# Performance work log

Measured on AMD Instinct MI355X. Metric: run time of the kernel, lower is better.

The kernel has to match this reference:

```python
import jax, jax.numpy as jnp
import numpy as np

N, E = 50000, 800000
IN_F, HID, HEADS, OUT_F = 128, 32, 4, 40
SLOPE = 0.2  # LeakyReLU negative slope (alpha)


def gatv2_layer(x, Wl, Wr, att, src, dst, n):
    # GATv2 (Brody et al.): score_ij = att . leakyrelu(Wl x_j + Wr x_i), message = Wl x_j
    H, F = att.shape
    gl = (x @ Wl).reshape(n, H, F)  # [N,H,F] source transform
    gr = (x @ Wr).reshape(n, H, F)  # [N,H,F] dest transform
    s = gl[src] + gr[dst]           # [E,H,F]
    e = jnp.where(s > 0, s, SLOPE * s)
    score = jnp.einsum('ehf,hf->eh', e, att)  # [E,H]
    m = jax.lax.stop_gradient(jax.ops.segment_max(score, dst, num_segments=n))
    a = jnp.exp(score - m[dst])
    denom = jax.ops.segment_sum(a, dst, num_segments=n)  # [N,H]
    w = a / (denom[dst] + 1e-16)                          # softmax over incoming edges
    out = jax.ops.segment_sum(w[:, :, None] * gl[src], dst, num_segments=n)  # [N,H,F]
    return out.reshape(n, H * F)


def setup_inputs() -> dict:
    key = jax.random.key(0)
    ks = jax.random.split(key, 12)
    d1 = HEADS * HID  # 128
    sc_in = 1.0 / np.sqrt(IN_F)
    sc_h = 1.0 / np.sqrt(d1)
    return {
        'x': jax.random.normal(ks[0], (N, IN_F), jnp.float32),
        'Wl1': jax.random.normal(ks[1], (IN_F, d1), jnp.float32) * sc_in,
        'Wr1': jax.random.normal(ks[2], (IN_F, d1), jnp.float32) * sc_in,
        'att1': jax.random.normal(ks[3], (HEADS, HID), jnp.float32) * (1.0 / np.sqrt(HID)),
        'Wl2': jax.random.normal(ks[4], (d1, d1), jnp.float32) * sc_h,
        'Wr2': jax.random.normal(ks[5], (d1, d1), jnp.float32) * sc_h,
        'att2': jax.random.normal(ks[6], (HEADS, HID), jnp.float32) * (1.0 / np.sqrt(HID)),
        'Wl3': jax.random.normal(ks[7], (d1, OUT_F), jnp.float32) * sc_h,
        'Wr3': jax.random.normal(ks[8], (d1, OUT_F), jnp.float32) * sc_h,
        'att3': jax.random.normal(ks[9], (1, OUT_F), jnp.float32) * (1.0 / np.sqrt(OUT_F)),
        'edge_index': jax.random.randint(ks[10], (2, E), 0, N, jnp.int64 if jax.config.jax_enable_x64 else jnp.int32),
    }


def reference(x, Wl1, Wr1, att1, Wl2, Wr2, att2, Wl3, Wr3, att3, edge_index):
    src, dst = edge_index[0], edge_index[1]
    h = jax.nn.elu(gatv2_layer(x, Wl1, Wr1, att1, src, dst, N))        # conv1 + ELU
    h = jax.nn.relu(gatv2_layer(h, Wl2, Wr2, att2, src, dst, N))       # hidden + ReLU (dropout off: eval)
    h = gatv2_layer(h, Wl3, Wr3, att3, src, dst, N)                    # conv2, 1 head
    return jax.nn.log_softmax(h, axis=1)
```

## Files before the change

### kernel.cpp

```cpp
#include <hip/hip_runtime.h>
#include <math.h>


#define TPB 256

typedef __attribute__((ext_vector_type(8))) short short8v;
typedef __attribute__((ext_vector_type(4))) float f32x4;

__device__ __forceinline__ short bf16rne(float v, float* recon) {
  unsigned u = __float_as_uint(v);
  unsigned r = (u + 0x7FFFu + ((u >> 16) & 1u)) >> 16;
  if (recon) *recon = __uint_as_float(r << 16);
  return (short)r;
}
__device__ __forceinline__ float bf2f(unsigned short u) {
  return __uint_as_float((unsigned)u << 16);
}

__global__ void k_prepW6(const float* __restrict__ s0, const float* __restrict__ s1,
                         const float* __restrict__ s2, const float* __restrict__ s3,
                         const float* __restrict__ s4, const float* __restrict__ s5,
                         short* __restrict__ wt) {
  int y = blockIdx.y;
  const float* W; short* hi; int M, Mp;
  if (y < 4) {
    W = (y == 0) ? s0 : (y == 1) ? s1 : (y == 2) ? s2 : s3;
    hi = wt + y * 32768; M = 128; Mp = 128;
  } else {
    W = (y == 4) ? s4 : s5;
    hi = wt + 131072 + (y - 4) * 12288; M = 40; Mp = 48;
  }
  short* lo = hi + 128 * Mp;
  int t = blockIdx.x * blockDim.x + threadIdx.x;
  if (t >= 128 * Mp) return;
  int m = t % Mp, k = t / Mp;
  float v = (m < M) ? W[k * M + m] : 0.f;
  float vh;
  short h = bf16rne(v, &vh);
  short l = bf16rne(v - vh, nullptr);
  hi[(size_t)m * 128 + k] = h;
  lo[(size_t)m * 128 + k] = l;
}

template <int ACT>
__device__ __forceinline__ void loadA(const float* __restrict__ x, int arow, int koff,
                                      short8v AH[4], short8v AL[4]) {
  const float4* px = reinterpret_cast<const float4*>(x + (size_t)arow * 128 + koff);
  float4 t[8];
#pragma unroll
  for (int k = 0; k < 4; ++k) {
    t[2 * k]     = px[k * 8];
    t[2 * k + 1] = px[k * 8 + 1];
  }
#pragma unroll
  for (int k = 0; k < 4; ++k) {
    float av[8] = {t[2 * k].x, t[2 * k].y, t[2 * k].z, t[2 * k].w,
                   t[2 * k + 1].x, t[2 * k + 1].y, t[2 * k + 1].z, t[2 * k + 1].w};
#pragma unroll
    for (int j = 0; j < 8; ++j) {
      float v = av[j];
      if (ACT == 1) v = v > 0.f ? v : (__expf(v) - 1.f);
      else if (ACT == 2) v = fmaxf(v, 0.f);
      float vh;
      AH[k][j] = bf16rne(v, &vh);
      AL[k][j] = bf16rne(v - vh, nullptr);
    }
  }
}

template <int ACT>
__global__ __launch_bounds__(256, 1) void k_gemm_mfma(
    const float* __restrict__ x,
    const short* __restrict__ blh, const short* __restrict__ bll,
    const short* __restrict__ brh, const short* __restrict__ brl,
    unsigned short* __restrict__ glh, float* __restrict__ gr, int n) {
  const int K = 128;
  int lane = threadIdx.x & 63;
  int w = threadIdx.x >> 6;
  int rbase = blockIdx.x * 64 + w * 16;
  int arow = rbase + (lane & 15);
  if (arow >= n) arow = n - 1;
  int koff = (lane >> 4) * 8;

  short8v AH[4], AL[4];
  loadA<ACT>(x, arow, koff, AH, AL);

  f32x4 acc[2][8];
#pragma unroll
  for (int m = 0; m < 2; ++m)
#pragma unroll
    for (int c = 0; c < 8; ++c) acc[m][c] = (f32x4)(0.f);

  int bbase = (lane & 15) * K + koff;

#define BOFF(IT) ((((IT) & 7) * 16 * K) + bbase + (((IT) >> 3) * 32))
  short8v cbh = *reinterpret_cast<const short8v*>(blh + BOFF(0));
  short8v cbl = *reinterpret_cast<const short8v*>(bll + BOFF(0));
  short8v cch = *reinterpret_cast<const short8v*>(brh + BOFF(0));
  short8v ccl = *reinterpret_cast<const short8v*>(brl + BOFF(0));
#pragma unroll
  for (int it = 0; it < 32; ++it) {
    const int k0i = it >> 3, c = it & 7;
    const int nit = (it + 1) & 31;
    short8v nbh = *reinterpret_cast<const short8v*>(blh + BOFF(nit));
    short8v nbl = *reinterpret_cast<const short8v*>(bll + BOFF(nit));
    short8v nch = *reinterpret_cast<const short8v*>(brh + BOFF(nit));
    short8v ncl = *reinterpret_cast<const short8v*>(brl + BOFF(nit));
    acc[0][c] = __builtin_amdgcn_mfma_f32_16x16x32_bf16(AH[k0i], cbh, acc[0][c], 0, 0, 0);
    acc[0][c] = __builtin_amdgcn_mfma_f32_16x16x32_bf16(AH[k0i], cbl, acc[0][c], 0, 0, 0);
    acc[0][c] = __builtin_amdgcn_mfma_f32_16x16x32_bf16(AL[k0i], cbh, acc[0][c], 0, 0, 0);
    acc[1][c] = __builtin_amdgcn_mfma_f32_16x16x32_bf16(AH[k0i], cch, acc[1][c], 0, 0, 0);
    acc[1][c] = __builtin_amdgcn_mfma_f32_16x16x32_bf16(AH[k0i], ccl, acc[1][c], 0, 0, 0);
    acc[1][c] = __builtin_amdgcn_mfma_f32_16x16x32_bf16(AL[k0i], cch, acc[1][c], 0, 0, 0);
    cbh = nbh; cbl = nbl; cch = nch; ccl = ncl;
  }
#undef BOFF

  int crow = rbase + (lane >> 4) * 4;
  int ccol = lane & 15;
#pragma unroll
  for (int c = 0; c < 8; ++c)
#pragma unroll
    for (int j = 0; j < 4; ++j) {
      int r = crow + j;
      if (r < n) {
        glh[(size_t)r * 128 + c * 16 + ccol] = (unsigned short)bf16rne(acc[0][c][j], nullptr);
        gr[(size_t)r * 128 + c * 16 + ccol] = acc[1][c][j];
      }
    }
}

template <int ACT>
__global__ __launch_bounds__(256, 1) void k_gemm_mfma3(
    const float* __restrict__ x,
    const short* __restrict__ blh, const short* __restrict__ bll,
    const short* __restrict__ brh, const short* __restrict__ brl,
    unsigned short* __restrict__ glh, float* __restrict__ gr, int n) {
  const int K = 128;
  int lane = threadIdx.x & 63;
  int w = threadIdx.x >> 6;
  int rbase = blockIdx.x * 64 + w * 16;
  int arow = rbase + (lane & 15);
  if (arow >= n) arow = n - 1;
  int koff = (lane >> 4) * 8;

  short8v AH[4], AL[4];
  loadA<ACT>(x, arow, koff, AH, AL);

  f32x4 acc[2][3];
#pragma unroll
  for (int m = 0; m < 2; ++m)
#pragma unroll
    for (int c = 0; c < 3; ++c) acc[m][c] = (f32x4)(0.f);

  int bbase = (lane & 15) * K + koff;

#define BOFF3(IT) ((((IT) % 3) * 16 * K) + bbase + (((IT) / 3) * 32))
  short8v cbh = *reinterpret_cast<const short8v*>(blh + BOFF3(0));
  short8v cbl = *reinterpret_cast<const short8v*>(bll + BOFF3(0));
  short8v cch = *reinterpret_cast<const short8v*>(brh + BOFF3(0));
  short8v ccl = *reinterpret_cast<const short8v*>(brl + BOFF3(0));
#pragma unroll
  for (int it = 0; it < 12; ++it) {
    const int k0i = it / 3, c = it % 3;
    const int nit = (it + 1) % 12;
    short8v nbh = *reinterpret_cast<const short8v*>(blh + BOFF3(nit));
    short8v nbl = *reinterpret_cast<const short8v*>(bll + BOFF3(nit));
    short8v nch = *reinterpret_cast<const short8v*>(brh + BOFF3(nit));
    short8v ncl = *reinterpret_cast<const short8v*>(brl + BOFF3(nit));
    acc[0][c] = __builtin_amdgcn_mfma_f32_16x16x32_bf16(AH[k0i], cbh, acc[0][c], 0, 0, 0);
    acc[0][c] = __builtin_amdgcn_mfma_f32_16x16x32_bf16(AH[k0i], cbl, acc[0][c], 0, 0, 0);
    acc[0][c] = __builtin_amdgcn_mfma_f32_16x16x32_bf16(AL[k0i], cbh, acc[0][c], 0, 0, 0);
    acc[1][c] = __builtin_amdgcn_mfma_f32_16x16x32_bf16(AH[k0i], cch, acc[1][c], 0, 0, 0);
    acc[1][c] = __builtin_amdgcn_mfma_f32_16x16x32_bf16(AH[k0i], ccl, acc[1][c], 0, 0, 0);
    acc[1][c] = __builtin_amdgcn_mfma_f32_16x16x32_bf16(AL[k0i], cch, acc[1][c], 0, 0, 0);
    cbh = nbh; cbl = nbl; cch = nch; ccl = ncl;
  }
#undef BOFF3

  int crow = rbase + (lane >> 4) * 4;
  int ccol = lane & 15;
#pragma unroll
  for (int c = 0; c < 3; ++c)
#pragma unroll
    for (int j = 0; j < 4; ++j) {
      int r = crow + j;
      int col = c * 16 + ccol;
      if (r < n && col < 40) {
        glh[(size_t)r * 40 + col] = (unsigned short)bf16rne(acc[0][c][j], nullptr);
        gr[(size_t)r * 40 + col] = acc[1][c][j];
      }
    }
}

__global__ void k_hist(const int* __restrict__ dst, int* __restrict__ cnt, int E) {
  int e = blockIdx.x * blockDim.x + threadIdx.x;
  if (e < E) atomicAdd(&cnt[dst[e]], 1);
}

__global__ void k_scan1(const int* __restrict__ cnt, int* __restrict__ rowptr,
                        int* __restrict__ bsum, int n) {
  __shared__ int wsum[16];
  int i = blockIdx.x * 1024 + threadIdx.x;
  int lane = threadIdx.x & 63, wid = threadIdx.x >> 6;
  int v = (i < n) ? cnt[i] : 0;
  int x = v;
#pragma unroll
  for (int off = 1; off < 64; off <<= 1) {
    int t = __shfl_up(x, off);
    if (lane >= off) x += t;
  }
  if (lane == 63) wsum[wid] = x;
  __syncthreads();
  if (wid == 0) {
    int wv = (lane < 16) ? wsum[lane] : 0;
#pragma unroll
    for (int off = 1; off < 16; off <<= 1) {
      int t = __shfl_up(wv, off);
      if (lane >= off) wv += t;
    }
    if (lane < 16) wsum[lane] = wv;
  }
  __syncthreads();
  int woff = wid ? wsum[wid - 1] : 0;
  if (i < n) rowptr[i] = woff + x - v;
  if (threadIdx.x == 1023) bsum[blockIdx.x] = wsum[15];
}

__global__ void k_scan2(const int* __restrict__ bsum, int* __restrict__ boff, int nb,
                        int* __restrict__ rowptr, int n) {
  int lane = threadIdx.x;
  int v = (lane < nb) ? bsum[lane] : 0;
  int x = v;
#pragma unroll
  for (int off = 1; off < 64; off <<= 1) {
    int t = __shfl_up(x, off);
    if (lane >= off) x += t;
  }
  if (lane < nb) boff[lane] = x - v;
  if (lane == 63) rowptr[n] = x;
}

__global__ void k_scan3(int* __restrict__ rowptr, const int* __restrict__ boff,
                        int* __restrict__ cur, int n) {
  int i = blockIdx.x * blockDim.x + threadIdx.x;
  if (i < n) {
    int r = rowptr[i] + boff[i >> 10];
    rowptr[i] = r;
    cur[i] = r;
  }
}

__global__ void k_fill(const int* __restrict__ src, const int* __restrict__ dst,
                       int* __restrict__ cur, int* __restrict__ csr_src, int E) {
  int e = blockIdx.x * blockDim.x + threadIdx.x;
  if (e >= E) return;
  int pos = atomicAdd(&cur[dst[e]], 1);
  csr_src[pos] = src[e];
}

__global__ void k_edge4(const unsigned short* __restrict__ glh, const float* __restrict__ gr,
                        const float* __restrict__ att, const int* __restrict__ rowptr,
                        const int* __restrict__ csr_src, float* __restrict__ out, int n) {
  int wid = (int)((blockIdx.x * blockDim.x + threadIdx.x) >> 6);
  if (wid >= n) return;
  int lane = threadIdx.x & 63;
  int p0 = rowptr[wid], p1 = rowptr[wid + 1];
  float2* po = reinterpret_cast<float2*>(out + (size_t)wid * 128);
  if (p1 <= p0) { po[lane] = make_float2(0.f, 0.f); return; }
  const float2 grv = reinterpret_cast<const float2*>(gr + (size_t)wid * 128)[lane];
  const float2 attv = reinterpret_cast<const float2*>(att)[lane];

  float l[8];
  float2 acc[8];
#pragma unroll
  for (int j = 0; j < 8; ++j) { l[j] = 0.f; acc[j] = make_float2(0.f, 0.f); }

#define LD(S) ({ ushort2 u_ = reinterpret_cast<const ushort2*>(glh + ((size_t)(S) << 7))[lane]; \
                 make_float2(bf2f(u_.x), bf2f(u_.y)); })
#define UPD4(J, G)                                                     \
  {                                                                    \
    float vx = (G).x + grv.x; vx = vx > 0.f ? vx : 0.2f * vx;          \
    float vy = (G).y + grv.y; vy = vy > 0.f ? vy : 0.2f * vy;          \
    float part = fmaf(vx, attv.x, vy * attv.y);                        \
    part += __shfl_xor(part, 1);                                       \
    part += __shfl_xor(part, 2);                                       \
    part += __shfl_xor(part, 4);                                       \
    part += __shfl_xor(part, 8);                                       \
    float w = __expf(part);                                            \
    l[J] += w;                                                         \
    acc[J].x = fmaf(w, (G).x, acc[J].x);                               \
    acc[J].y = fmaf(w, (G).y, acc[J].y);                               \
  }

  for (int base = p0; base < p1; base += 64) {
    int nv = p1 - base; if (nv > 64) nv = 64;
    int sv = (base + lane < p1) ? csr_src[base + lane] : 0;
    int i = 0;
    for (; i + 8 <= nv; i += 8) {
      int s0 = __shfl(sv, i + 0), s1 = __shfl(sv, i + 1);
      int s2 = __shfl(sv, i + 2), s3 = __shfl(sv, i + 3);
      int s4 = __shfl(sv, i + 4), s5 = __shfl(sv, i + 5);
      int s6 = __shfl(sv, i + 6), s7 = __shfl(sv, i + 7);
      float2 g0 = LD(s0), g1 = LD(s1), g2 = LD(s2), g3 = LD(s3);
      float2 g4 = LD(s4), g5 = LD(s5), g6 = LD(s6), g7 = LD(s7);
      UPD4(0, g0); UPD4(1, g1); UPD4(2, g2); UPD4(3, g3);
      UPD4(4, g4); UPD4(5, g5); UPD4(6, g6); UPD4(7, g7);
    }
    for (; i < nv; ++i) {
      int s0 = __shfl(sv, i);
      float2 g0 = LD(s0);
      UPD4(0, g0);
    }
  }
#undef UPD4
#undef LD

  float lt = 0.f;
  float2 at = make_float2(0.f, 0.f);
#pragma unroll
  for (int j = 0; j < 8; ++j) {
    lt += l[j];
    at.x += acc[j].x;
    at.y += acc[j].y;
  }
  float inv = 1.f / (lt + 1e-16f);
  po[lane] = make_float2(at.x * inv, at.y * inv);
}

__global__ void k_edge1ls(const unsigned short* __restrict__ glh, const float* __restrict__ gr,
                          const float* __restrict__ att, const int* __restrict__ rowptr,
                          const int* __restrict__ csr_src, float* __restrict__ outf, int n) {
  int wv = (int)((blockIdx.x * blockDim.x + threadIdx.x) >> 6);
  int lane = threadIdx.x & 63;
  int half = lane >> 5, hl = lane & 31;
  int d = wv * 2 + half;
  if (d >= n) d = n - 1;
  bool fok = hl < 20;
  float2 grv = fok ? reinterpret_cast<const float2*>(gr + (size_t)d * 40)[hl]
                   : make_float2(0.f, 0.f);
  float2 attv = fok ? reinterpret_cast<const float2*>(att)[hl] : make_float2(0.f, 0.f);
  int p0 = rowptr[d], p1 = rowptr[d + 1];
  int ec = p1 - p0;
  int nch = (ec + 31) >> 5;
  { int o = __shfl_xor(nch, 32); nch = nch > o ? nch : o; }

  float l0 = 0.f, l1 = 0.f;
  float2 a0 = make_float2(0.f, 0.f), a1 = make_float2(0.f, 0.f);

  for (int c = 0; c < nch; ++c) {
    int base = p0 + c * 32;
    int sv = (base + hl < p1) ? csr_src[base + hl] : 0;
    int nv = p1 - base;
    nv = nv < 0 ? 0 : (nv > 32 ? 32 : nv);
    int nvmax = nv;
    { int o = __shfl_xor(nvmax, 32); nvmax = nvmax > o ? nvmax : o; }
    for (int i = 0; i < nvmax; i += 2) {
      int s0 = __shfl(sv, (half << 5) + i);
      int s1 = __shfl(sv, (half << 5) + i + 1);
      bool v0 = i < nv, v1 = (i + 1) < nv;
      float2 g0 = make_float2(0.f, 0.f), g1 = make_float2(0.f, 0.f);
      if (v0 && fok) { ushort2 u = reinterpret_cast<const ushort2*>(glh + (size_t)s0 * 40)[hl]; g0 = make_float2(bf2f(u.x), bf2f(u.y)); }
      if (v1 && fok) { ushort2 u = reinterpret_cast<const ushort2*>(glh + (size_t)s1 * 40)[hl]; g1 = make_float2(bf2f(u.x), bf2f(u.y)); }
      float e0x = g0.x + grv.x; e0x = e0x > 0.f ? e0x : 0.2f * e0x;
      float e0y = g0.y + grv.y; e0y = e0y > 0.f ? e0y : 0.2f * e0y;
      float pt0 = fmaf(e0x, attv.x, e0y * attv.y);
      float e1x = g1.x + grv.x; e1x = e1x > 0.f ? e1x : 0.2f * e1x;
      float e1y = g1.y + grv.y; e1y = e1y > 0.f ? e1y : 0.2f * e1y;
      float pt1 = fmaf(e1x, attv.x, e1y * attv.y);
#pragma unroll
      for (int o = 1; o < 32; o <<= 1) {
        pt0 += __shfl_xor(pt0, o);
        pt1 += __shfl_xor(pt1, o);
      }
      float w0 = v0 ? __expf(pt0) : 0.f;
      float w1 = v1 ? __expf(pt1) : 0.f;
      l0 += w0;
      a0.x = fmaf(w0, g0.x, a0.x);
      a0.y = fmaf(w0, g0.y, a0.y);
      l1 += w1;
      a1.x = fmaf(w1, g1.x, a1.x);
      a1.y = fmaf(w1, g1.y, a1.y);
    }
  }

  float lt = l0 + l1;
  float inv = 1.f / (lt + 1e-16f);
  float ox = (a0.x + a1.x) * inv;
  float oy = (a0.y + a1.y) * inv;

  float mx = fok ? fmaxf(ox, oy) : -INFINITY;
#pragma unroll
  for (int o = 1; o < 32; o <<= 1) mx = fmaxf(mx, __shfl_xor(mx, o));
  float ex = fok ? (__expf(ox - mx) + __expf(oy - mx)) : 0.f;
  float sm = ex;
#pragma unroll
  for (int o = 1; o < 32; o <<= 1) sm += __shfl_xor(sm, o);
  float lg = logf(sm);
  if (fok) {
    float2* po = reinterpret_cast<float2*>(outf + (size_t)d * 40);
    po[hl] = make_float2(ox - mx - lg, oy - mx - lg);
  }
}

static inline int cdiv(long long a, int b) { return (int)((a + b - 1) / b); }

extern "C" void kernel_launch(void* const* d_in, const int* in_sizes, int n_in,
                              void* d_out, int out_size, void* d_ws, size_t ws_size,
                              hipStream_t stream) {
  const float* x    = (const float*)d_in[0];
  const float* Wl1  = (const float*)d_in[1];
  const float* Wr1  = (const float*)d_in[2];
  const float* att1 = (const float*)d_in[3];
  const float* Wl2  = (const float*)d_in[4];
  const float* Wr2  = (const float*)d_in[5];
  const float* att2 = (const float*)d_in[6];
  const float* Wl3  = (const float*)d_in[7];
  const float* Wr3  = (const float*)d_in[8];
  const float* att3 = (const float*)d_in[9];
  const int*   ei   = (const int*)d_in[10];

  const int N = in_sizes[0] / 128;
  const int E = in_sizes[10] / 2;
  const int* src = ei;
  const int* dst = ei + E;

  short* wt = (short*)d_ws;
  short* wl1h = wt +      0;  short* wl1l = wt +  16384;
  short* wr1h = wt +  32768;  short* wr1l = wt +  49152;
  short* wl2h = wt +  65536;  short* wl2l = wt +  81920;
  short* wr2h = wt +  98304;  short* wr2l = wt + 114688;
  short* wl3h = wt + 131072;  short* wl3l = wt + 137216;
  short* wr3h = wt + 143360;  short* wr3l = wt + 149504;

  float* fbase  = (float*)d_ws + 77824;
  float* bufA   = fbase;
  float* bufGR  = bufA + (size_t)N * 128;
  unsigned short* bufGLh = (unsigned short*)(bufGR + (size_t)N * 128);
  int*   cnt    = (int*)(bufGR + (size_t)N * 128 + (size_t)N * 64);
  int*   rowptr = cnt + N;
  int*   cur    = rowptr + N + 1;
  int*   csrS   = cur + N;
  int*   bsum   = csrS + E;
  int*   boff   = bsum + 64;

  float* outf = (float*)d_out;

  const int nb = cdiv(N, 1024);

  hipMemsetAsync(cnt, 0, (size_t)N * sizeof(int), stream);
  k_hist<<<cdiv(E, TPB), TPB, 0, stream>>>(dst, cnt, E);
  k_prepW6<<<dim3(64, 6), TPB, 0, stream>>>(Wl1, Wr1, Wl2, Wr2, Wl3, Wr3, wt);
  k_scan1<<<nb, 1024, 0, stream>>>(cnt, rowptr, bsum, N);
  k_scan2<<<1, 64, 0, stream>>>(bsum, boff, nb, rowptr, N);
  k_scan3<<<cdiv(N, TPB), TPB, 0, stream>>>(rowptr, boff, cur, N);
  k_fill<<<cdiv(E, TPB), TPB, 0, stream>>>(src, dst, cur, csrS, E);

  k_gemm_mfma<0><<<cdiv(N, 64), 256, 0, stream>>>(x, wl1h, wl1l, wr1h, wr1l, bufGLh, bufGR, N);
  k_edge4<<<cdiv(N, 4), TPB, 0, stream>>>(bufGLh, bufGR, att1, rowptr, csrS, bufA, N);

  k_gemm_mfma<1><<<cdiv(N, 64), 256, 0, stream>>>(bufA, wl2h, wl2l, wr2h, wr2l, bufGLh, bufGR, N);
  k_edge4<<<cdiv(N, 4), TPB, 0, stream>>>(bufGLh, bufGR, att2, rowptr, csrS, bufA, N);

  k_gemm_mfma3<2><<<cdiv(N, 64), 256, 0, stream>>>(bufA, wl3h, wl3l, wr3h, wr3l, bufGLh, bufGR, N);
  k_edge1ls<<<cdiv(cdiv(N, 2), 4), TPB, 0, stream>>>(bufGLh, bufGR, att3, rowptr, csrS, outf, N);
}
```

Baseline: 518.1 us.

## Split GEMM work across waves by output columns instead of rows

The node-transform GEMM kernels now give each block 16 rows, and each wave computes a slice of output column tiles (2 of 8 tiles for 128-wide, one 16-col tile per wave for the 40-wide layer with 192 threads). This cuts accumulator registers per wave and drops the occupancy-1 launch bound, so more waves can be resident to hide latency. In exchange each A row block is loaded and split into bf16 hi/lo by every wave (redundant loads and conversion), and the grid is four times larger.

```diff
diff --git a/kernel.cpp b/kernel.cpp
--- a/kernel.cpp
+++ b/kernel.cpp
@@ -69,7 +69,7 @@
 }
 
 template <int ACT>
-__global__ __launch_bounds__(256, 1) void k_gemm_mfma(
+__global__ __launch_bounds__(256) void k_gemm_mfma(
     const float* __restrict__ x,
     const short* __restrict__ blh, const short* __restrict__ bll,
     const short* __restrict__ brh, const short* __restrict__ brl,
@@ -77,7 +77,7 @@
   const int K = 128;
   int lane = threadIdx.x & 63;
   int w = threadIdx.x >> 6;
-  int rbase = blockIdx.x * 64 + w * 16;
+  int rbase = blockIdx.x * 16;
   int arow = rbase + (lane & 15);
   if (arow >= n) arow = n - 1;
   int koff = (lane >> 4) * 8;
@@ -85,33 +85,34 @@
   short8v AH[4], AL[4];
   loadA<ACT>(x, arow, koff, AH, AL);
 
-  f32x4 acc[2][8];
+  f32x4 acc[2][2];
 #pragma unroll
   for (int m = 0; m < 2; ++m)
 #pragma unroll
-    for (int c = 0; c < 8; ++c) acc[m][c] = (f32x4)(0.f);
+    for (int c = 0; c < 2; ++c) acc[m][c] = (f32x4)(0.f);
 
   int bbase = (lane & 15) * K + koff;
-
-#define BOFF(IT) ((((IT) & 7) * 16 * K) + bbase + (((IT) >> 3) * 32))
+  const int cb = w * 2;
+
+#define BOFF(IT) (((cb + ((IT) & 1)) * 16 * K) + bbase + (((IT) >> 1) * 32))
   short8v cbh = *reinterpret_cast<const short8v*>(blh + BOFF(0));
   short8v cbl = *reinterpret_cast<const short8v*>(bll + BOFF(0));
   short8v cch = *reinterpret_cast<const short8v*>(brh + BOFF(0));
   short8v ccl = *reinterpret_cast<const short8v*>(brl + BOFF(0));
 #pragma unroll
-  for (int it = 0; it < 32; ++it) {
-    const int k0i = it >> 3, c = it & 7;
-    const int nit = (it + 1) & 31;
+  for (int it = 0; it < 8; ++it) {
+    const int k0i = it >> 1, ci = it & 1;
+    const int nit = (it + 1) & 7;
     short8v nbh = *reinterpret_cast<const short8v*>(blh + BOFF(nit));
     short8v nbl = *reinterpret_cast<const short8v*>(bll + BOFF(nit));
     short8v nch = *reinterpret_cast<const short8v*>(brh + BOFF(nit));
     short8v ncl = *reinterpret_cast<const short8v*>(brl + BOFF(nit));
-    acc[0][c] = __builtin_amdgcn_mfma_f32_16x16x32_bf16(AH[k0i], cbh, acc[0][c], 0, 0, 0);
-    acc[0][c] = __builtin_amdgcn_mfma_f32_16x16x32_bf16(AH[k0i], cbl, acc[0][c], 0, 0, 0);
-    acc[0][c] = __builtin_amdgcn_mfma_f32_16x16x32_bf16(AL[k0i], cbh, acc[0][c], 0, 0, 0);
-    acc[1][c] = __builtin_amdgcn_mfma_f32_16x16x32_bf16(AH[k0i], cch, acc[1][c], 0, 0, 0);
-    acc[1][c] = __builtin_amdgcn_mfma_f32_16x16x32_bf16(AH[k0i], ccl, acc[1][c], 0, 0, 0);
-    acc[1][c] = __builtin_amdgcn_mfma_f32_16x16x32_bf16(AL[k0i], cch, acc[1][c], 0, 0, 0);
+    acc[0][ci] = __builtin_amdgcn_mfma_f32_16x16x32_bf16(AH[k0i], cbh, acc[0][ci], 0, 0, 0);
+    acc[0][ci] = __builtin_amdgcn_mfma_f32_16x16x32_bf16(AH[k0i], cbl, acc[0][ci], 0, 0, 0);
+    acc[0][ci] = __builtin_amdgcn_mfma_f32_16x16x32_bf16(AL[k0i], cbh, acc[0][ci], 0, 0, 0);
+    acc[1][ci] = __builtin_amdgcn_mfma_f32_16x16x32_bf16(AH[k0i], cch, acc[1][ci], 0, 0, 0);
+    acc[1][ci] = __builtin_amdgcn_mfma_f32_16x16x32_bf16(AH[k0i], ccl, acc[1][ci], 0, 0, 0);
+    acc[1][ci] = __builtin_amdgcn_mfma_f32_16x16x32_bf16(AL[k0i], cch, acc[1][ci], 0, 0, 0);
     cbh = nbh; cbl = nbl; cch = nch; ccl = ncl;
   }
 #undef BOFF
@@ -119,19 +120,21 @@
   int crow = rbase + (lane >> 4) * 4;
   int ccol = lane & 15;
 #pragma unroll
-  for (int c = 0; c < 8; ++c)
+  for (int ci = 0; ci < 2; ++ci) {
+    int c = cb + ci;
 #pragma unroll
     for (int j = 0; j < 4; ++j) {
       int r = crow + j;
       if (r < n) {
-        glh[(size_t)r * 128 + c * 16 + ccol] = (unsigned short)bf16rne(acc[0][c][j], nullptr);
-        gr[(size_t)r * 128 + c * 16 + ccol] = acc[1][c][j];
+        glh[(size_t)r * 128 + c * 16 + ccol] = (unsigned short)bf16rne(acc[0][ci][j], nullptr);
+        gr[(size_t)r * 128 + c * 16 + ccol] = acc[1][ci][j];
       }
     }
+  }
 }
 
 template <int ACT>
-__global__ __launch_bounds__(256, 1) void k_gemm_mfma3(
+__global__ __launch_bounds__(192) void k_gemm_mfma3(
     const float* __restrict__ x,
     const short* __restrict__ blh, const short* __restrict__ bll,
     const short* __restrict__ brh, const short* __restrict__ brl,
@@ -139,7 +142,7 @@
   const int K = 128;
   int lane = threadIdx.x & 63;
   int w = threadIdx.x >> 6;
-  int rbase = blockIdx.x * 64 + w * 16;
+  int rbase = blockIdx.x * 16;
   int arow = rbase + (lane & 15);
   if (arow >= n) arow = n - 1;
   int koff = (lane >> 4) * 8;
@@ -147,50 +150,39 @@
   short8v AH[4], AL[4];
   loadA<ACT>(x, arow, koff, AH, AL);
 
-  f32x4 acc[2][3];
-#pragma unroll
-  for (int m = 0; m < 2; ++m)
-#pragma unroll
-    for (int c = 0; c < 3; ++c) acc[m][c] = (f32x4)(0.f);
-
-  int bbase = (lane & 15) * K + koff;
-
-#define BOFF3(IT) ((((IT) % 3) * 16 * K) + bbase + (((IT) / 3) * 32))
-  short8v cbh = *reinterpret_cast<const short8v*>(blh + BOFF3(0));
-  short8v cbl = *reinterpret_cast<const short8v*>(bll + BOFF3(0));
-  short8v cch = *reinterpret_cast<const short8v*>(brh + BOFF3(0));
-  short8v ccl = *reinterpret_cast<const short8v*>(brl + BOFF3(0));
-#pragma unroll
-  for (int it = 0; it < 12; ++it) {
-    const int k0i = it / 3, c = it % 3;
-    const int nit = (it + 1) % 12;
-    short8v nbh = *reinterpret_cast<const short8v*>(blh + BOFF3(nit));
-    short8v nbl = *reinterpret_cast<const short8v*>(bll + BOFF3(nit));
-    short8v nch = *reinterpret_cast<const short8v*>(brh + BOFF3(nit));
-    short8v ncl = *reinterpret_cast<const short8v*>(brl + BOFF3(nit));
-    acc[0][c] = __builtin_amdgcn_mfma_f32_16x16x32_bf16(AH[k0i], cbh, acc[0][c], 0, 0, 0);
-    acc[0][c] = __builtin_amdgcn_mfma_f32_16x16x32_bf16(AH[k0i], cbl, acc[0][c], 0, 0, 0);
-    acc[0][c] = __builtin_amdgcn_mfma_f32_16x16x32_bf16(AL[k0i], cbh, acc[0][c], 0, 0, 0);
-    acc[1][c] = __builtin_amdgcn_mfma_f32_16x16x32_bf16(AH[k0i], cch, acc[1][c], 0, 0, 0);
-    acc[1][c] = __builtin_amdgcn_mfma_f32_16x16x32_bf16(AH[k0i], ccl, acc[1][c], 0, 0, 0);
-    acc[1][c] = __builtin_amdgcn_mfma_f32_16x16x32_bf16(AL[k0i], cch, acc[1][c], 0, 0, 0);
-    cbh = nbh; cbl = nbl; cch = nch; ccl = ncl;
-  }
-#undef BOFF3
+  int bbase = w * 16 * K + (lane & 15) * K + koff;
+
+  short8v Bh[4], Bl[4], Ch[4], Cl[4];
+#pragma unroll
+  for (int k = 0; k < 4; ++k) {
+    Bh[k] = *reinterpret_cast<const short8v*>(blh + bbase + k * 32);
+    Bl[k] = *reinterpret_cast<const short8v*>(bll + bbase + k * 32);
+    Ch[k] = *reinterpret_cast<const short8v*>(brh + bbase + k * 32);
+    Cl[k] = *reinterpret_cast<const short8v*>(brl + bbase + k * 32);
+  }
+
+  f32x4 accL = (f32x4)(0.f), accR = (f32x4)(0.f);
+#pragma unroll
+  for (int k = 0; k < 4; ++k) {
+    accL = __builtin_amdgcn_mfma_f32_16x16x32_bf16(AH[k], Bh[k], accL, 0, 0, 0);
+    accL = __builtin_amdgcn_mfma_f32_16x16x32_bf16(AH[k], Bl[k], accL, 0, 0, 0);
+    accL = __builtin_amdgcn_mfma_f32_16x16x32_bf16(AL[k], Bh[k], accL, 0, 0, 0);
+    accR = __builtin_amdgcn_mfma_f32_16x16x32_bf16(AH[k], Ch[k], accR, 0, 0, 0);
+    accR = __builtin_amdgcn_mfma_f32_16x16x32_bf16(AH[k], Cl[k], accR, 0, 0, 0);
+    accR = __builtin_amdgcn_mfma_f32_16x16x32_bf16(AL[k], Ch[k], accR, 0, 0, 0);
+  }
 
   int crow = rbase + (lane >> 4) * 4;
   int ccol = lane & 15;
-#pragma unroll
-  for (int c = 0; c < 3; ++c)
-#pragma unroll
-    for (int j = 0; j < 4; ++j) {
-      int r = crow + j;
-      int col = c * 16 + ccol;
-      if (r < n && col < 40) {
-        glh[(size_t)r * 40 + col] = (unsigned short)bf16rne(acc[0][c][j], nullptr);
-        gr[(size_t)r * 40 + col] = acc[1][c][j];
-      }
-    }
+  int col = w * 16 + ccol;
+#pragma unroll
+  for (int j = 0; j < 4; ++j) {
+    int r = crow + j;
+    if (r < n && col < 40) {
+      glh[(size_t)r * 40 + col] = (unsigned short)bf16rne(accL[j], nullptr);
+      gr[(size_t)r * 40 + col] = accR[j];
+    }
+  }
 }
 
 __global__ void k_hist(const int* __restrict__ dst, int* __restrict__ cnt, int E) {
@@ -456,12 +448,12 @@
   k_scan3<<<cdiv(N, TPB), TPB, 0, stream>>>(rowptr, boff, cur, N);
   k_fill<<<cdiv(E, TPB), TPB, 0, stream>>>(src, dst, cur, csrS, E);
 
-  k_gemm_mfma<0><<<cdiv(N, 64), 256, 0, stream>>>(x, wl1h, wl1l, wr1h, wr1l, bufGLh, bufGR, N);
+  k_gemm_mfma<0><<<cdiv(N, 16), 256, 0, stream>>>(x, wl1h, wl1l, wr1h, wr1l, bufGLh, bufGR, N);
   k_edge4<<<cdiv(N, 4), TPB, 0, stream>>>(bufGLh, bufGR, att1, rowptr, csrS, bufA, N);
 
-  k_gemm_mfma<1><<<cdiv(N, 64), 256, 0, stream>>>(bufA, wl2h, wl2l, wr2h, wr2l, bufGLh, bufGR, N);
+  k_gemm_mfma<1><<<cdiv(N, 16), 256, 0, stream>>>(bufA, wl2h, wl2l, wr2h, wr2l, bufGLh, bufGR, N);
   k_edge4<<<cdiv(N, 4), TPB, 0, stream>>>(bufGLh, bufGR, att2, rowptr, csrS, bufA, N);
 
-  k_gemm_mfma3<2><<<cdiv(N, 64), 256, 0, stream>>>(bufA, wl3h, wl3l, wr3h, wr3l, bufGLh, bufGR, N);
+  k_gemm_mfma3<2><<<cdiv(N, 16), 192, 0, stream>>>(bufA, wl3h, wl3l, wr3h, wr3l, bufGLh, bufGR, N);
   k_edge1ls<<<cdiv(cdiv(N, 2), 4), TPB, 0, stream>>>(bufGLh, bufGR, att3, rowptr, csrS, outf, N);
 }
```

Result: faster. 507.1 us (-2.1%).
